# Kernel optimization log

Hardware: AMD Instinct MI355X
Metric: run time of the kernel (lower is better)

The kernel has to match this reference:

```python
import jax, jax.numpy as jnp
import numpy as np

ORDER_WEIGHT = 1.0
RELATION_WEIGHT = 0.5

B, N, R = 32, 384, 16


def setup_inputs() -> dict:
    key = jax.random.key(0)
    k1, k2, k3, k4, k5, k6 = jax.random.split(key, 6)
    order_logits = jax.random.normal(k1, (B, N, N), dtype=jnp.float32)
    relation_logits = jax.random.normal(k2, (B, N, N, R), dtype=jnp.float32)
    reading_orders = jax.random.randint(k3, (B, N), 0, N)
    # parent_ids in [-1, N): -1 means root (no relation loss contribution)
    parent_ids = jax.random.randint(k4, (B, N), -1, N)
    # relations in [-1, R): -1 means ignored
    relations = jax.random.randint(k5, (B, N), -1, R)
    region_mask = jax.random.randint(k6, (B, N), 0, 2).astype(jnp.bool_)
    return {
        "order_logits": order_logits,
        "relation_logits": relation_logits,
        "reading_orders": reading_orders,
        "parent_ids": parent_ids,
        "relations": relations,
        "region_mask": region_mask,
    }


def reference(order_logits, relation_logits, reading_orders, parent_ids, relations, region_mask):
    b, n = reading_orders.shape
    # ---- pairwise reading-order BCE loss ----
    targets = (reading_orders[:, :, None] < reading_orders[:, None, :]).astype(order_logits.dtype)
    valid_mask = region_mask[:, :, None] & region_mask[:, None, :]
    valid_mask = valid_mask & (~jnp.eye(n, dtype=jnp.bool_))[None, :, :]
    # stable BCE-with-logits: softplus(x) - x*t
    bce = jnp.logaddexp(jnp.zeros_like(order_logits), order_logits) - order_logits * targets
    vm = valid_mask.astype(order_logits.dtype)
    order_loss = (bce * vm).sum() / jnp.maximum(valid_mask.sum(), 1).astype(order_logits.dtype)

    # ---- relation cross-entropy loss (vectorized gather) ----
    rel_valid = region_mask & (parent_ids >= 0) & (parent_ids < n) & (relations >= 0)
    p = jnp.clip(parent_ids, 0, n - 1)                       # [B, N]
    rel = jnp.clip(relations, 0, relation_logits.shape[-1] - 1)
    b_idx = jnp.arange(b)[:, None]
    i_idx = jnp.arange(n)[None, :]
    pair_logits = relation_logits[b_idx, p, i_idx]           # [B, N, R]
    ce = jax.nn.logsumexp(pair_logits, axis=-1) - jnp.take_along_axis(
        pair_logits, rel[:, :, None], axis=-1)[:, :, 0]      # [B, N]
    rv = rel_valid.astype(ce.dtype)
    relation_loss = (ce * rv).sum() / jnp.maximum(rel_valid.sum(), 1).astype(ce.dtype)

    total_loss = ORDER_WEIGHT * order_loss + RELATION_WEIGHT * relation_loss
    return total_loss, order_loss, relation_loss
```

## Files before the change

### kernel.cpp

```cpp
#include <hip/hip_runtime.h>

#define BB 32
#define NN 384
#define RR 16
#define GRID_MAIN 768
#define BLK 256

__device__ __forceinline__ float softplus_f(float x) {
    return fmaxf(x, 0.0f) + log1pf(expf(-fabsf(x)));
}

__device__ __forceinline__ void blockReduce4(float& f0, int& c0, float& f1, int& c1) {
    #pragma unroll
    for (int off = 32; off > 0; off >>= 1) {
        f0 += __shfl_down(f0, off, 64);
        c0 += __shfl_down(c0, off, 64);
        f1 += __shfl_down(f1, off, 64);
        c1 += __shfl_down(c1, off, 64);
    }
    __shared__ float sf0[16], sf1[16];
    __shared__ int   sc0[16], sc1[16];
    int lane = threadIdx.x & 63;
    int wave = threadIdx.x >> 6;
    if (lane == 0) { sf0[wave] = f0; sc0[wave] = c0; sf1[wave] = f1; sc1[wave] = c1; }
    __syncthreads();
    int nw = blockDim.x >> 6;
    if (wave == 0) {
        f0 = (lane < nw) ? sf0[lane] : 0.0f;
        c0 = (lane < nw) ? sc0[lane] : 0;
        f1 = (lane < nw) ? sf1[lane] : 0.0f;
        c1 = (lane < nw) ? sc1[lane] : 0;
        #pragma unroll
        for (int off = 32; off > 0; off >>= 1) {
            f0 += __shfl_down(f0, off, 64);
            c0 += __shfl_down(c0, off, 64);
            f1 += __shfl_down(f1, off, 64);
            c1 += __shfl_down(c1, off, 64);
        }
    }
}

__global__ __launch_bounds__(BLK) void main_loss_kernel(
        const float* __restrict__ order_logits,
        const float* __restrict__ relation_logits,
        const int* __restrict__ reading_orders,
        const int* __restrict__ parent_ids,
        const int* __restrict__ relations,
        const unsigned char* __restrict__ region_mask,
        float4* __restrict__ ws) {
    const int N4 = NN / 4;
    const int total4 = BB * NN * N4;
    const int gid = blockIdx.x * BLK + threadIdx.x;

    float oSum = 0.0f; int oCnt = 0;
    for (int idx = gid; idx < total4; idx += GRID_MAIN * BLK) {
        int j4 = (idx % N4) * 4;
        int bi = idx / N4;
        if (!region_mask[bi]) continue;
        int i  = bi % NN;
        int bBase = bi - i;
        int ro_i = reading_orders[bi];
        float4 x4 = ((const float4*)order_logits)[idx];
        #pragma unroll
        for (int k = 0; k < 4; ++k) {
            int j = j4 + k;
            float x = (&x4.x)[k];
            if (region_mask[bBase + j] && (i != j)) {
                float t = (ro_i < reading_orders[bBase + j]) ? 1.0f : 0.0f;
                oSum += softplus_f(x) - x * t;
                oCnt++;
            }
        }
    }

    float rSum = 0.0f; int rCnt = 0;
    if (gid < BB * NN) {
        int b = gid / NN, i = gid % NN;
        int p = parent_ids[gid];
        int r = relations[gid];
        if (region_mask[gid] && p >= 0 && p < NN && r >= 0) {
            const float4* row =
                (const float4*)(relation_logits + ((size_t)(b * NN + p) * NN + i) * RR);
            float v[RR];
            float4 a0 = row[0], a1 = row[1], a2 = row[2], a3 = row[3];
            v[0]=a0.x;  v[1]=a0.y;  v[2]=a0.z;  v[3]=a0.w;
            v[4]=a1.x;  v[5]=a1.y;  v[6]=a1.z;  v[7]=a1.w;
            v[8]=a2.x;  v[9]=a2.y;  v[10]=a2.z; v[11]=a2.w;
            v[12]=a3.x; v[13]=a3.y; v[14]=a3.z; v[15]=a3.w;
            float m = v[0];
            #pragma unroll
            for (int k = 1; k < RR; ++k) m = fmaxf(m, v[k]);
            float s = 0.0f;
            #pragma unroll
            for (int k = 0; k < RR; ++k) s += expf(v[k] - m);
            rSum = m + logf(s) - v[r];
            rCnt = 1;
        }
    }

    blockReduce4(oSum, oCnt, rSum, rCnt);
    if (threadIdx.x == 0) {
        float4 out;
        out.x = oSum;
        out.y = __int_as_float(oCnt);
        out.z = rSum;
        out.w = __int_as_float(rCnt);
        ws[blockIdx.x] = out;
    }
}

__global__ __launch_bounds__(BLK) void finalize_kernel(const float4* __restrict__ ws,
                                                       float* __restrict__ out) {
    float oSum = 0.0f, rSum = 0.0f;
    int oCnt = 0, rCnt = 0;
    for (int i = threadIdx.x; i < GRID_MAIN; i += BLK) {
        float4 v = ws[i];
        oSum += v.x;
        oCnt += __float_as_int(v.y);
        rSum += v.z;
        rCnt += __float_as_int(v.w);
    }
    blockReduce4(oSum, oCnt, rSum, rCnt);
    if (threadIdx.x == 0) {
        float order_loss = oSum / (float)(oCnt > 1 ? oCnt : 1);
        float rel_loss   = rSum / (float)(rCnt > 1 ? rCnt : 1);
        out[0] = 1.0f * order_loss + 0.5f * rel_loss;
        out[1] = order_loss;
        out[2] = rel_loss;
    }
}

extern "C" void kernel_launch(void* const* d_in, const int* in_sizes, int n_in,
                              void* d_out, int out_size, void* d_ws, size_t ws_size,
                              hipStream_t stream) {
    const float* order_logits    = (const float*)d_in[0];
    const float* relation_logits = (const float*)d_in[1];
    const int* reading_orders    = (const int*)d_in[2];
    const int* parent_ids        = (const int*)d_in[3];
    const int* relations         = (const int*)d_in[4];
    const unsigned char* region_mask = (const unsigned char*)d_in[5];
    float* out  = (float*)d_out;
    float4* ws4 = (float4*)d_ws;

    main_loss_kernel<<<GRID_MAIN, BLK, 0, stream>>>(
        order_logits, relation_logits, reading_orders, parent_ids, relations,
        region_mask, ws4);
    finalize_kernel<<<1, BLK, 0, stream>>>(ws4, out);
}
```

Baseline: 348.8 us.

## Use one float4 per thread with vectorized mask loads and fast exp/log intrinsics

Grid size changes from a fixed 768-block grid-stride loop to one float4 per thread (4608 blocks). Per-j region mask and reading-order values now come from a single uchar4 and int4 load instead of scalar loads. Softplus and logsumexp now use the hardware exp2/log intrinsics instead of libm calls, and the relation target is picked with a select rather than a dynamic index. The larger grid makes the finalize kernel sum more partials, and the fast intrinsics trade a little accuracy for speed.

New measurement: 349.4 us. No clear change (+0.2%).

```diff
diff --git a/kernel.cpp b/kernel.cpp
--- a/kernel.cpp
+++ b/kernel.cpp
@@ -3,11 +3,18 @@
 #define BB 32
 #define NN 384
 #define RR 16
-#define GRID_MAIN 768
+#define N4 (NN / 4)
+#define TOTAL4 (BB * NN * N4)
 #define BLK 256
+#define GRID_MAIN (TOTAL4 / BLK)
 
-__device__ __forceinline__ float softplus_f(float x) {
-    return fmaxf(x, 0.0f) + log1pf(expf(-fabsf(x)));
+#define LOG2E 1.4426950408889634f
+#define LN2   0.6931471805599453f
+
+__device__ __forceinline__ float softplus_fast(float x) {
+    float a = fabsf(x);
+    float e = __builtin_amdgcn_exp2f(-a * LOG2E);
+    return fmaxf(x, 0.0f) + LN2 * __builtin_amdgcn_logf(1.0f + e);
 }
 
 __device__ __forceinline__ void blockReduce4(float& f0, int& c0, float& f1, int& c1) {
@@ -48,27 +55,30 @@
         const int* __restrict__ relations,
         const unsigned char* __restrict__ region_mask,
         float4* __restrict__ ws) {
-    const int N4 = NN / 4;
-    const int total4 = BB * NN * N4;
     const int gid = blockIdx.x * BLK + threadIdx.x;
 
     float oSum = 0.0f; int oCnt = 0;
-    for (int idx = gid; idx < total4; idx += GRID_MAIN * BLK) {
-        int j4 = (idx % N4) * 4;
-        int bi = idx / N4;
-        if (!region_mask[bi]) continue;
-        int i  = bi % NN;
-        int bBase = bi - i;
-        int ro_i = reading_orders[bi];
-        float4 x4 = ((const float4*)order_logits)[idx];
-        #pragma unroll
-        for (int k = 0; k < 4; ++k) {
-            int j = j4 + k;
-            float x = (&x4.x)[k];
-            if (region_mask[bBase + j] && (i != j)) {
-                float t = (ro_i < reading_orders[bBase + j]) ? 1.0f : 0.0f;
-                oSum += softplus_f(x) - x * t;
-                oCnt++;
+    {
+        int j4 = (gid % N4) * 4;
+        int bi = gid / N4;
+        if (region_mask[bi]) {
+            int i  = bi % NN;
+            int bBase = bi - i;
+            int ro_i = reading_orders[bi];
+            float4 x4 = ((const float4*)order_logits)[gid];
+            uchar4 m4 = *(const uchar4*)(region_mask + bBase + j4);
+            int4  ro4 = *(const int4*)(reading_orders + bBase + j4);
+            #pragma unroll
+            for (int k = 0; k < 4; ++k) {
+                int j = j4 + k;
+                float x  = (&x4.x)[k];
+                int   mj = (&m4.x)[k];
+                int  roj = (&ro4.x)[k];
+                if (mj && (i != j)) {
+                    float t = (ro_i < roj) ? 1.0f : 0.0f;
+                    oSum += softplus_fast(x) - x * t;
+                    oCnt++;
+                }
             }
         }
     }
@@ -81,8 +91,8 @@
         if (region_mask[gid] && p >= 0 && p < NN && r >= 0) {
             const float4* row =
                 (const float4*)(relation_logits + ((size_t)(b * NN + p) * NN + i) * RR);
+            float4 a0 = row[0], a1 = row[1], a2 = row[2], a3 = row[3];
             float v[RR];
-            float4 a0 = row[0], a1 = row[1], a2 = row[2], a3 = row[3];
             v[0]=a0.x;  v[1]=a0.y;  v[2]=a0.z;  v[3]=a0.w;
             v[4]=a1.x;  v[5]=a1.y;  v[6]=a1.z;  v[7]=a1.w;
             v[8]=a2.x;  v[9]=a2.y;  v[10]=a2.z; v[11]=a2.w;
@@ -90,10 +100,13 @@
             float m = v[0];
             #pragma unroll
             for (int k = 1; k < RR; ++k) m = fmaxf(m, v[k]);
-            float s = 0.0f;
+            float s = 0.0f, tgt = 0.0f;
             #pragma unroll
-            for (int k = 0; k < RR; ++k) s += expf(v[k] - m);
-            rSum = m + logf(s) - v[r];
+            for (int k = 0; k < RR; ++k) {
+                s += __builtin_amdgcn_exp2f((v[k] - m) * LOG2E);
+                tgt = (k == r) ? v[k] : tgt;
+            }
+            rSum = m + LN2 * __builtin_amdgcn_logf(s) - tgt;
             rCnt = 1;
         }
     }
```
